# Optimization experiments

Hardware: AMD Instinct MI355X
Metric: run time of the kernel (lower is better)

## Reference

```python
import jax, jax.numpy as jnp
import numpy as np

S, B, IN, H = 512, 128, 256, 512  # seq_len, batch, input_size, hidden_size


def setup_inputs() -> dict:
    key = jax.random.key(0)
    ks = jax.random.split(key, 17)
    def p(k, shape):
        return jax.random.normal(k, shape, dtype=jnp.float32) * 0.05
    inp = {
        "x": jax.random.normal(ks[0], (S, B, IN), dtype=jnp.float32),
        "h0": jnp.zeros((1, B, H), dtype=jnp.float32),
        "c0": jnp.zeros((1, B, H), dtype=jnp.float32),
    }
    # gates: f=forget, i=input, o=output, g=cell candidate
    for j, n in enumerate(["f", "i", "o", "g"]):
        inp[f"W{n}"] = p(ks[1 + 4 * j], (H, IN))
        inp[f"bW{n}"] = p(ks[2 + 4 * j], (H,))
        inp[f"U{n}"] = p(ks[3 + 4 * j], (H, H))
        inp[f"bU{n}"] = p(ks[4 + 4 * j], (H,))
    return inp


def reference(x, h0, c0, Wf, bWf, Uf, bUf, Wi, bWi, Ui, bUi,
              Wo, bWo, Uo, bUo, Wg, bWg, Ug, bUg):
    # Fuse the 4 input projections and 4 recurrent projections into single GEMMs.
    # Math is identical to applying each Linear separately.
    Wcat = jnp.concatenate([Wf, Wi, Wo, Wg], axis=0)      # [4H, IN]
    bcat = jnp.concatenate([bWf + bUf, bWi + bUi, bWo + bUo, bWg + bUg])  # [4H]
    Ucat = jnp.concatenate([Uf, Ui, Uo, Ug], axis=0)      # [4H, H]
    hd = h0.shape[-1]
    # Precompute input-dependent gate pre-activations for all timesteps.
    xg = jnp.einsum('sbi,gi->sbg', x, Wcat) + bcat        # [S, B, 4H]

    def step(carry, xg_t):
        h, c = carry
        g = xg_t + h @ Ucat.T                             # [B, 4H]
        f = jax.nn.sigmoid(g[..., :hd])
        i = jax.nn.sigmoid(g[..., hd:2 * hd])
        o = jax.nn.sigmoid(g[..., 2 * hd:3 * hd])
        cand = jnp.tanh(g[..., 3 * hd:])
        c = f * c + i * cand
        h = o * jnp.tanh(c)
        return (h, c), h

    (h, c), h_seq = jax.lax.scan(step, (h0[-1], c0[-1]), xg)
    return h_seq, h, c
```

## Files before the change

### kernel.cpp

```cpp
#include <hip/hip_runtime.h>
#include <hip/hip_cooperative_groups.h>

namespace cg = cooperative_groups;


#define SQ   512
#define BB   128
#define IN_  256
#define HH   512
#define RG   8
#define CGN  32
#define RINGHALF (BB * HH)
#define RING_OFF 1024

typedef float    f32x4 __attribute__((ext_vector_type(4)));
typedef short    s16x8 __attribute__((ext_vector_type(8)));
typedef unsigned u32x4 __attribute__((ext_vector_type(4)));

struct P {
  const float *x, *h0, *c0;
  const float *W[4], *bW[4], *U[4], *bU[4];
  float* out;
  unsigned* ring;
  int mode;
};

__device__ __forceinline__ unsigned f2b(float f) {
  unsigned u = __float_as_uint(f);
  return (u + 0x7FFFu + ((u >> 16) & 1u)) >> 16;
}
__device__ __forceinline__ float sigm(float x) { return 1.f / (1.f + __expf(-x)); }
__device__ __forceinline__ float tanh_(float x) {
  float e = __expf(-2.f * fabsf(x));
  float t = (1.f - e) / (1.f + e);
  return copysignf(t, x);
}
__device__ __forceinline__ u32x4 pack8(f32x4 a, f32x4 b) {
  u32x4 d;
  d.x = f2b(a.x) | (f2b(a.y) << 16);
  d.y = f2b(a.z) | (f2b(a.w) << 16);
  d.z = f2b(b.x) | (f2b(b.y) << 16);
  d.w = f2b(b.z) | (f2b(b.w) << 16);
  return d;
}

#define LOAD8_LLC(c0_,c1_,c2_,c3_,c4_,c5_,c6_,c7_,ptr_)                      \
  asm volatile(                                                              \
    "global_load_dwordx4 %0, %8, off sc0 sc1\n\t"                            \
    "global_load_dwordx4 %1, %8, off offset:256 sc0 sc1\n\t"                 \
    "global_load_dwordx4 %2, %8, off offset:512 sc0 sc1\n\t"                 \
    "global_load_dwordx4 %3, %8, off offset:768 sc0 sc1\n\t"                 \
    "global_load_dwordx4 %4, %8, off offset:1024 sc0 sc1\n\t"                \
    "global_load_dwordx4 %5, %8, off offset:1280 sc0 sc1\n\t"                \
    "global_load_dwordx4 %6, %8, off offset:1536 sc0 sc1\n\t"                \
    "global_load_dwordx4 %7, %8, off offset:1792 sc0 sc1\n\t"                \
    "s_waitcnt vmcnt(0)"                                                     \
    : "=&v"(c0_), "=&v"(c1_), "=&v"(c2_), "=&v"(c3_),                        \
      "=&v"(c4_), "=&v"(c5_), "=&v"(c6_), "=&v"(c7_)                         \
    : "v"(ptr_) : "memory")

__global__ void __launch_bounds__(256, 1) lstm_all(P p) {
  __shared__ unsigned short Hs[16][512];
  __shared__ unsigned short Xs[2][16][256];
  __shared__ float gbuf[4][16][17];

  const int tid = threadIdx.x;
  const int bid = blockIdx.x;
  const int r   = bid & 7;
  const int cgi = bid >> 3;
  const int rb  = r * 16;
  const int hcb = cgi * 16;

  const int w   = tid >> 6;
  const int l   = tid & 63;
  const int l16 = l & 15;
  const int lk  = l >> 4;
  const int row16 = tid >> 4;
  const int n16   = tid & 15;

  unsigned* ring = p.ring;

  const int col = hcb + l16;
  s16x8 bfrag[24];
#pragma unroll
  for (int kk = 0; kk < 24; ++kk) {
    int k = kk * 32 + lk * 8;
    const float* src = (kk < 8) ? (p.W[w] + (size_t)col * IN_ + k)
                                : (p.U[w] + (size_t)col * HH + (k - IN_));
    f32x4 a = *(const f32x4*)src;
    f32x4 b = *(const f32x4*)(src + 4);
    s16x8 v;
    v[0]=(short)f2b(a.x); v[1]=(short)f2b(a.y); v[2]=(short)f2b(a.z); v[3]=(short)f2b(a.w);
    v[4]=(short)f2b(b.x); v[5]=(short)f2b(b.y); v[6]=(short)f2b(b.z); v[7]=(short)f2b(b.w);
    bfrag[kk] = v;
  }
  const float bias = p.bW[w][col] + p.bU[w][col];
  float cval = p.c0[(size_t)(rb + row16) * HH + hcb + n16];

  const int wswz = (row16 & 7) << 4;
  const int rswz = (l16 & 7) << 4;
  char* HsB = (char*)&Hs[0][0];
  char* XsB = (char*)&Xs[0][0][0];

  f32x4 xg0, xg1, xg2, xg3;
  {
    const float* xs = p.x + (size_t)(rb + row16) * IN_ + n16 * 16;
    xg0 = *(const f32x4*)(xs);
    xg1 = *(const f32x4*)(xs + 4);
    xg2 = *(const f32x4*)(xs + 8);
    xg3 = *(const f32x4*)(xs + 12);
  }

  for (int t = 0; t < SQ; ++t) {
    {
      char* xrow = XsB + (t & 1) * 8192 + row16 * 512;
      *(u32x4*)(xrow + ((n16 * 32)      ^ wswz)) = pack8(xg0, xg1);
      *(u32x4*)(xrow + ((n16 * 32 + 16) ^ wswz)) = pack8(xg2, xg3);
      if (t + 1 < SQ) {
        const float* xs = p.x + ((size_t)(t + 1) * BB + rb + row16) * IN_ + n16 * 16;
        xg0 = *(const f32x4*)(xs);
        xg1 = *(const f32x4*)(xs + 4);
        xg2 = *(const f32x4*)(xs + 8);
        xg3 = *(const f32x4*)(xs + 12);
      }
    }

    char* hrow = HsB + row16 * 1024;
    if (t == 0) {
      const float* src = p.h0 + (size_t)(rb + row16) * HH + n16 * 4;
#pragma unroll
      for (int cc = 0; cc < 8; ++cc) {
        f32x4 v = *(const f32x4*)(src + cc * 64);
        unsigned lo = f2b(v.x) | (f2b(v.y) << 16);
        unsigned hi = f2b(v.z) | (f2b(v.w) << 16);
        int boff = ((cc * 128 + n16 * 8) ^ wswz);
        *(uint2*)(hrow + boff) = make_uint2(lo, hi);
      }
    } else if (p.mode == 0) {
      const unsigned* hb = ring + (((t - 1) & 1) ? RINGHALF : 0)
                         + (size_t)(rb + row16) * HH + n16 * 4;
      u32x4 c0,c1,c2,c3,c4,c5,c6,c7;
      const unsigned tg = (unsigned)t;
#define TAGOK(v) (((v).x >> 16) == tg && ((v).y >> 16) == tg && \
                  ((v).z >> 16) == tg && ((v).w >> 16) == tg)
      int spin = 0;
      for (;;) {
        LOAD8_LLC(c0,c1,c2,c3,c4,c5,c6,c7,hb);
        if (TAGOK(c0) && TAGOK(c1) && TAGOK(c2) && TAGOK(c3) &&
            TAGOK(c4) && TAGOK(c5) && TAGOK(c6) && TAGOK(c7)) break;
        if (++spin > (1 << 16)) break;
        if (spin > 8) __builtin_amdgcn_s_sleep(1);
      }
#undef TAGOK
      u32x4 cv[8] = {c0,c1,c2,c3,c4,c5,c6,c7};
#pragma unroll
      for (int cc = 0; cc < 8; ++cc) {
        unsigned lo = (cv[cc].x & 0xFFFFu) | (cv[cc].y << 16);
        unsigned hi = (cv[cc].z & 0xFFFFu) | (cv[cc].w << 16);
        int boff = ((cc * 128 + n16 * 8) ^ wswz);
        *(uint2*)(hrow + boff) = make_uint2(lo, hi);
      }
    } else {
      cg::this_grid().sync();
      const float* hp = p.out + ((size_t)(t - 1) * BB + rb + row16) * HH + n16 * 4;
      u32x4 a0,a1,a2,a3,a4,a5,a6,a7;
      LOAD8_LLC(a0,a1,a2,a3,a4,a5,a6,a7,hp);
      u32x4 av[8] = {a0,a1,a2,a3,a4,a5,a6,a7};
#pragma unroll
      for (int cc = 0; cc < 8; ++cc) {
        unsigned lo = f2b(__uint_as_float(av[cc].x)) | (f2b(__uint_as_float(av[cc].y)) << 16);
        unsigned hi = f2b(__uint_as_float(av[cc].z)) | (f2b(__uint_as_float(av[cc].w)) << 16);
        int boff = ((cc * 128 + n16 * 8) ^ wswz);
        *(uint2*)(hrow + boff) = make_uint2(lo, hi);
      }
    }
    __syncthreads();

    f32x4 acc0 = { bias, bias, bias, bias };
    f32x4 acc1 = { 0.f, 0.f, 0.f, 0.f };
    const char* xr = XsB + (t & 1) * 8192 + l16 * 512;
    const char* hr = HsB + l16 * 1024;
#pragma unroll
    for (int kp = 0; kp < 8; kp += 2) {
      s16x8 a0 = *(const s16x8*)(xr + ((kp * 64 + lk * 16)       ^ rswz));
      s16x8 a1 = *(const s16x8*)(xr + (((kp + 1) * 64 + lk * 16) ^ rswz));
      acc0 = __builtin_amdgcn_mfma_f32_16x16x32_bf16(a0, bfrag[kp],     acc0, 0, 0, 0);
      acc1 = __builtin_amdgcn_mfma_f32_16x16x32_bf16(a1, bfrag[kp + 1], acc1, 0, 0, 0);
    }
#pragma unroll
    for (int kp = 0; kp < 16; kp += 2) {
      s16x8 a0 = *(const s16x8*)(hr + ((kp * 64 + lk * 16)       ^ rswz));
      s16x8 a1 = *(const s16x8*)(hr + (((kp + 1) * 64 + lk * 16) ^ rswz));
      acc0 = __builtin_amdgcn_mfma_f32_16x16x32_bf16(a0, bfrag[8 + kp], acc0, 0, 0, 0);
      acc1 = __builtin_amdgcn_mfma_f32_16x16x32_bf16(a1, bfrag[9 + kp], acc1, 0, 0, 0);
    }

#pragma unroll
    for (int rr = 0; rr < 4; ++rr) {
      float v = acc0[rr] + acc1[rr];
      v = (w < 3) ? sigm(v) : tanh_(v);
      gbuf[w][lk * 4 + rr][l16] = v;
    }
    __syncthreads();

    float f = gbuf[0][row16][n16];
    float i = gbuf[1][row16][n16];
    float o = gbuf[2][row16][n16];
    float g = gbuf[3][row16][n16];
    cval = f * cval + i * g;
    float h = o * tanh_(cval);

    size_t oidx = ((size_t)t * BB + rb + row16) * HH + hcb + n16;
    if (p.mode == 0) {
      unsigned tw = ((unsigned)(t + 1) << 16) | f2b(h);
      unsigned* dst = ring + ((t & 1) ? RINGHALF : 0)
                    + (size_t)(rb + row16) * HH + hcb + n16;
      asm volatile("global_store_dword %0, %1, off sc0 sc1"
                   :: "v"(dst), "v"(tw) : "memory");
      __builtin_nontemporal_store(h, p.out + oidx);
    } else {
      asm volatile("global_store_dword %0, %1, off sc0 sc1"
                   :: "v"(p.out + oidx), "v"(h) : "memory");
      asm volatile("s_waitcnt vmcnt(0)" ::: "memory");
    }
    if (t == SQ - 1) {
      size_t base = (size_t)SQ * BB * HH;
      size_t idx2 = (size_t)(rb + row16) * HH + hcb + n16;
      p.out[base + idx2] = h;
      p.out[base + (size_t)BB * HH + idx2] = cval;
    }
  }
}

extern "C" void kernel_launch(void* const* d_in, const int* in_sizes, int n_in,
                              void* d_out, int out_size, void* d_ws, size_t ws_size,
                              hipStream_t stream) {
  P p;
  p.x  = (const float*)d_in[0];
  p.h0 = (const float*)d_in[1];
  p.c0 = (const float*)d_in[2];
  for (int g = 0; g < 4; ++g) {
    p.W[g]  = (const float*)d_in[3 + 4 * g];
    p.bW[g] = (const float*)d_in[4 + 4 * g];
    p.U[g]  = (const float*)d_in[5 + 4 * g];
    p.bU[g] = (const float*)d_in[6 + 4 * g];
  }
  p.out = (float*)d_out;

  const size_t need = (size_t)(RING_OFF + 2 * BB * HH) * sizeof(unsigned);
  const bool ws_ok = (d_ws != nullptr) && (ws_size >= need);
  p.mode = ws_ok ? 0 : 2;
  p.ring = ws_ok ? ((unsigned*)d_ws + RING_OFF) : nullptr;
  if (ws_ok) hipMemsetAsync(d_ws, 0, need, stream);

  void* args[] = { &p };
  hipError_t e = hipLaunchCooperativeKernel((const void*)lstm_all,
                                            dim3(RG * CGN), dim3(256),
                                            args, 0, stream);
  if (e != hipSuccess) {
    hipLaunchKernelGGL(lstm_all, dim3(RG * CGN), dim3(256), 0, stream, p);
  }
}
```

Measured before the change: 1.298 ms.

## Overlap ring h-load latency with input-projection MFMAs and prefetch x two steps ahead

The ring-buffer loads of the previous hidden state are now issued at the start of each step without waiting. The x-part MFMAs, which do not depend on h, run while those loads are in flight. The x tile is staged one step ahead in shared memory (first tile written before the loop) and the global x load moves two steps ahead. The bf16 unpack of ring entries uses a single v_perm instead of mask/shift/or. This hides the cross-block communication latency behind independent compute, at the cost of more register pressure and a reshuffled shared-memory double-buffer schedule.

```diff
diff --git a/kernel.cpp b/kernel.cpp
--- a/kernel.cpp
+++ b/kernel.cpp
@@ -43,6 +43,23 @@
   d.w = f2b(b.z) | (f2b(b.w) << 16);
   return d;
 }
+__device__ __forceinline__ unsigned mergelo(unsigned d0, unsigned d1) {
+  return __builtin_amdgcn_perm(d1, d0, 0x05040100u);
+}
+
+#define ISSUE8_LLC(c0_,c1_,c2_,c3_,c4_,c5_,c6_,c7_,ptr_)                     \
+  asm volatile(                                                              \
+    "global_load_dwordx4 %0, %8, off sc0 sc1\n\t"                            \
+    "global_load_dwordx4 %1, %8, off offset:256 sc0 sc1\n\t"                 \
+    "global_load_dwordx4 %2, %8, off offset:512 sc0 sc1\n\t"                 \
+    "global_load_dwordx4 %3, %8, off offset:768 sc0 sc1\n\t"                 \
+    "global_load_dwordx4 %4, %8, off offset:1024 sc0 sc1\n\t"                \
+    "global_load_dwordx4 %5, %8, off offset:1280 sc0 sc1\n\t"                \
+    "global_load_dwordx4 %6, %8, off offset:1536 sc0 sc1\n\t"                \
+    "global_load_dwordx4 %7, %8, off offset:1792 sc0 sc1"                    \
+    : "=&v"(c0_), "=&v"(c1_), "=&v"(c2_), "=&v"(c3_),                        \
+      "=&v"(c4_), "=&v"(c5_), "=&v"(c6_), "=&v"(c7_)                         \
+    : "v"(ptr_) : "memory")
 
 #define LOAD8_LLC(c0_,c1_,c2_,c3_,c4_,c5_,c6_,c7_,ptr_)                      \
   asm volatile(                                                              \
@@ -102,27 +119,48 @@
   char* HsB = (char*)&Hs[0][0];
   char* XsB = (char*)&Xs[0][0][0];
 
+  {
+    const float* xs = p.x + (size_t)(rb + row16) * IN_ + n16 * 16;
+    f32x4 a0 = *(const f32x4*)(xs);
+    f32x4 b0 = *(const f32x4*)(xs + 4);
+    f32x4 a1 = *(const f32x4*)(xs + 8);
+    f32x4 b1 = *(const f32x4*)(xs + 12);
+    char* xrow = XsB + row16 * 512;
+    *(u32x4*)(xrow + ((n16 * 32)      ^ wswz)) = pack8(a0, b0);
+    *(u32x4*)(xrow + ((n16 * 32 + 16) ^ wswz)) = pack8(a1, b1);
+  }
   f32x4 xg0, xg1, xg2, xg3;
   {
-    const float* xs = p.x + (size_t)(rb + row16) * IN_ + n16 * 16;
+    const float* xs = p.x + ((size_t)1 * BB + rb + row16) * IN_ + n16 * 16;
     xg0 = *(const f32x4*)(xs);
     xg1 = *(const f32x4*)(xs + 4);
     xg2 = *(const f32x4*)(xs + 8);
     xg3 = *(const f32x4*)(xs + 12);
   }
+  __syncthreads();
 
   for (int t = 0; t < SQ; ++t) {
-    {
-      char* xrow = XsB + (t & 1) * 8192 + row16 * 512;
+    u32x4 c0, c1, c2, c3, c4, c5, c6, c7;
+    const unsigned* hb = ring + (((t - 1) & 1) ? RINGHALF : 0)
+                       + (size_t)(rb + row16) * HH + n16 * 4;
+    const bool ringstep = (t > 0) && (p.mode == 0);
+    if (ringstep) { ISSUE8_LLC(c0, c1, c2, c3, c4, c5, c6, c7, hb); }
+
+    if (t + 1 < SQ) {
+      char* xrow = XsB + ((t + 1) & 1) * 8192 + row16 * 512;
       *(u32x4*)(xrow + ((n16 * 32)      ^ wswz)) = pack8(xg0, xg1);
       *(u32x4*)(xrow + ((n16 * 32 + 16) ^ wswz)) = pack8(xg2, xg3);
-      if (t + 1 < SQ) {
-        const float* xs = p.x + ((size_t)(t + 1) * BB + rb + row16) * IN_ + n16 * 16;
-        xg0 = *(const f32x4*)(xs);
-        xg1 = *(const f32x4*)(xs + 4);
-        xg2 = *(const f32x4*)(xs + 8);
-        xg3 = *(const f32x4*)(xs + 12);
-      }
+    }
+
+    f32x4 acc0 = { bias, bias, bias, bias };
+    f32x4 acc1 = { 0.f, 0.f, 0.f, 0.f };
+    const char* xr = XsB + (t & 1) * 8192 + l16 * 512;
+#pragma unroll
+    for (int kp = 0; kp < 8; kp += 2) {
+      s16x8 a0 = *(const s16x8*)(xr + ((kp * 64 + lk * 16)       ^ rswz));
+      s16x8 a1 = *(const s16x8*)(xr + (((kp + 1) * 64 + lk * 16) ^ rswz));
+      acc0 = __builtin_amdgcn_mfma_f32_16x16x32_bf16(a0, bfrag[kp],     acc0, 0, 0, 0);
+      acc1 = __builtin_amdgcn_mfma_f32_16x16x32_bf16(a1, bfrag[kp + 1], acc1, 0, 0, 0);
     }
 
     char* hrow = HsB + row16 * 1024;
@@ -137,35 +175,35 @@
         *(uint2*)(hrow + boff) = make_uint2(lo, hi);
       }
     } else if (p.mode == 0) {
-      const unsigned* hb = ring + (((t - 1) & 1) ? RINGHALF : 0)
-                         + (size_t)(rb + row16) * HH + n16 * 4;
-      u32x4 c0,c1,c2,c3,c4,c5,c6,c7;
+      asm volatile("s_waitcnt vmcnt(0)" ::: "memory");
+      __builtin_amdgcn_sched_barrier(0);
       const unsigned tg = (unsigned)t;
 #define TAGOK(v) (((v).x >> 16) == tg && ((v).y >> 16) == tg && \
                   ((v).z >> 16) == tg && ((v).w >> 16) == tg)
       int spin = 0;
       for (;;) {
-        LOAD8_LLC(c0,c1,c2,c3,c4,c5,c6,c7,hb);
         if (TAGOK(c0) && TAGOK(c1) && TAGOK(c2) && TAGOK(c3) &&
             TAGOK(c4) && TAGOK(c5) && TAGOK(c6) && TAGOK(c7)) break;
         if (++spin > (1 << 16)) break;
         if (spin > 8) __builtin_amdgcn_s_sleep(1);
+        LOAD8_LLC(c0, c1, c2, c3, c4, c5, c6, c7, hb);
+        __builtin_amdgcn_sched_barrier(0);
       }
 #undef TAGOK
-      u32x4 cv[8] = {c0,c1,c2,c3,c4,c5,c6,c7};
+      u32x4 cv[8] = {c0, c1, c2, c3, c4, c5, c6, c7};
 #pragma unroll
       for (int cc = 0; cc < 8; ++cc) {
-        unsigned lo = (cv[cc].x & 0xFFFFu) | (cv[cc].y << 16);
-        unsigned hi = (cv[cc].z & 0xFFFFu) | (cv[cc].w << 16);
+        uint2 u = make_uint2(mergelo(cv[cc].x, cv[cc].y),
+                             mergelo(cv[cc].z, cv[cc].w));
         int boff = ((cc * 128 + n16 * 8) ^ wswz);
-        *(uint2*)(hrow + boff) = make_uint2(lo, hi);
+        *(uint2*)(hrow + boff) = u;
       }
     } else {
       cg::this_grid().sync();
       const float* hp = p.out + ((size_t)(t - 1) * BB + rb + row16) * HH + n16 * 4;
-      u32x4 a0,a1,a2,a3,a4,a5,a6,a7;
-      LOAD8_LLC(a0,a1,a2,a3,a4,a5,a6,a7,hp);
-      u32x4 av[8] = {a0,a1,a2,a3,a4,a5,a6,a7};
+      u32x4 a0, a1, a2, a3, a4, a5, a6, a7;
+      LOAD8_LLC(a0, a1, a2, a3, a4, a5, a6, a7, hp);
+      u32x4 av[8] = {a0, a1, a2, a3, a4, a5, a6, a7};
 #pragma unroll
       for (int cc = 0; cc < 8; ++cc) {
         unsigned lo = f2b(__uint_as_float(av[cc].x)) | (f2b(__uint_as_float(av[cc].y)) << 16);
@@ -174,19 +212,17 @@
         *(uint2*)(hrow + boff) = make_uint2(lo, hi);
       }
     }
+
+    if (t + 2 < SQ) {
+      const float* xs = p.x + ((size_t)(t + 2) * BB + rb + row16) * IN_ + n16 * 16;
+      xg0 = *(const f32x4*)(xs);
+      xg1 = *(const f32x4*)(xs + 4);
+      xg2 = *(const f32x4*)(xs + 8);
+      xg3 = *(const f32x4*)(xs + 12);
+    }
     __syncthreads();
 
-    f32x4 acc0 = { bias, bias, bias, bias };
-    f32x4 acc1 = { 0.f, 0.f, 0.f, 0.f };
-    const char* xr = XsB + (t & 1) * 8192 + l16 * 512;
     const char* hr = HsB + l16 * 1024;
-#pragma unroll
-    for (int kp = 0; kp < 8; kp += 2) {
-      s16x8 a0 = *(const s16x8*)(xr + ((kp * 64 + lk * 16)       ^ rswz));
-      s16x8 a1 = *(const s16x8*)(xr + (((kp + 1) * 64 + lk * 16) ^ rswz));
-      acc0 = __builtin_amdgcn_mfma_f32_16x16x32_bf16(a0, bfrag[kp],     acc0, 0, 0, 0);
-      acc1 = __builtin_amdgcn_mfma_f32_16x16x32_bf16(a1, bfrag[kp + 1], acc1, 0, 0, 0);
-    }
 #pragma unroll
     for (int kp = 0; kp < 16; kp += 2) {
       s16x8 a0 = *(const s16x8*)(hr + ((kp * 64 + lk * 16)       ^ rswz));
```

After: 1.999 ms. +54.1%, slower.
